# Optimization experiments

Measured on AMD Instinct MI355X. Metric: run time of the kernel, lower is better.

Reference implementation:

```python
import jax, jax.numpy as jnp
import numpy as np

V = 50000
E = 640000
DIM = 128
NUM_EDGE_TYPES = 32


def setup_inputs() -> dict:
    key = jax.random.key(0)
    ks = jax.random.split(key, 8)
    return {
        "node_values": jax.random.normal(ks[0], (V, DIM), dtype=jnp.float32),
        "edge_src": jax.random.randint(ks[1], (E,), 0, V, dtype=jnp.int32),
        "edge_dest": jax.random.randint(ks[2], (E,), 0, V, dtype=jnp.int32),
        "edge_cls": jax.random.randint(ks[3], (E,), 0, NUM_EDGE_TYPES, dtype=jnp.int32),
        "W_src": jax.random.normal(ks[4], (DIM, DIM), dtype=jnp.float32) / np.sqrt(DIM),
        "b_src": jnp.zeros((DIM,), dtype=jnp.float32),
        "W_dest": jax.random.normal(ks[5], (DIM, DIM), dtype=jnp.float32) / np.sqrt(DIM),
        "b_dest": jnp.zeros((DIM,), dtype=jnp.float32),
        "edge_emb": jax.random.normal(ks[6], (NUM_EDGE_TYPES, DIM), dtype=jnp.float32),
    }


def reference(node_values, edge_src, edge_dest, edge_cls, W_src, b_src, W_dest, b_dest, edge_emb):
    # Dense projections over all nodes, then gather per edge (matches tf.gather(dense(...), idx))
    src_proj = node_values @ W_src + b_src    # [V, dim]
    dest_proj = node_values @ W_dest + b_dest  # [V, dim]
    # Per-edge fused message: gather src, gather dest, edge-class embedding lookup, add, relu
    msgs = jax.nn.relu(src_proj[edge_src] + dest_proj[edge_dest] + edge_emb[edge_cls])  # [E, dim]
    # Scatter-reduce messages onto destination nodes
    out = jax.ops.segment_sum(msgs, edge_dest, num_segments=V)  # [V, dim]
    return out
```

## Files before the change

kernel.cpp:

```cpp
#include <hip/hip_runtime.h>


#define V 50000
#define E 640000
#define DIM 128
#define NXCD 8
#define NBIN_R 50
#define BINW 125
#define NBINS 400
#define BINCAP 2048
#define QCAP 384
#define NCHUNK 256
#define CSRN 2500
#define EC4 625
#define NPROJ 782
#define NFUSED 1038

typedef __bf16 bf16x8 __attribute__((ext_vector_type(8)));
typedef float  f32x4  __attribute__((ext_vector_type(4)));
typedef float  f32x2  __attribute__((ext_vector_type(2)));

__device__ __forceinline__ float bf2f(unsigned int u16) {
    union { unsigned int i; float f; } c; c.i = u16 << 16; return c.f;
}
__device__ __forceinline__ unsigned int f2bf(float f) {
    union { float f; unsigned int i; } c; c.f = f;
    unsigned int u = c.i;
    return (u + 0x7FFFu + ((u >> 16) & 1u)) >> 16;
}

__global__ __launch_bounds__(256) void mp_setup(
    const float* __restrict__ Ws, const float* __restrict__ Wd,
    const float* __restrict__ emb,
    unsigned short* __restrict__ Wpk, unsigned short* __restrict__ embB,
    int* __restrict__ binCnt)
{
    int tid = blockIdx.x * 256 + threadIdx.x;
    int mat  = tid >> 11;
    int rem  = tid & 2047;
    int ct   = rem >> 8;
    int kt   = (rem >> 6) & 3;
    int lane = rem & 63;
    const float* W = mat ? Wd : Ws;
    int n  = ct * 16 + (lane & 15);
    int k0 = kt * 32 + (lane >> 4) * 8;
    unsigned short* dst = Wpk + (size_t)tid * 8;
    #pragma unroll
    for (int j = 0; j < 8; ++j) dst[j] = (unsigned short)f2bf(W[(k0 + j) * DIM + n]);
    embB[tid] = (unsigned short)f2bf(emb[tid]);
    if (tid < NBINS) binCnt[tid] = 0;
}

__global__ __launch_bounds__(256) void mp_fused(
    const int* __restrict__ ed, const int* __restrict__ es, const int* __restrict__ ec,
    int* __restrict__ binCnt, int* __restrict__ binbuf,
    const float* __restrict__ x, const unsigned short* __restrict__ Wpk,
    const float* __restrict__ bs, const float* __restrict__ bd,
    unsigned char* __restrict__ ps8, unsigned short* __restrict__ pdB)
{
    __shared__ float stage[4][16 * 132];

    const int b = blockIdx.x;
    const int t = threadIdx.x;
    const bool isBin = ((b & 3) == 3) && (b < 1024);

    if (isBin) {
        int* base  = (int*)&stage[0][0];
        int* hist  = base;
        int* lofs  = base + 400;
        int* lcur  = base + 801;
        int* gbase = base + 1201;
        int* csr   = base + 1601;
        unsigned short* sbin = (unsigned short*)(base + 4101);

        const int c = b >> 2;

        for (int i = t; i < NBINS; i += 256) hist[i] = 0;

        int4 DV[3], SV[3], CV[3];
        {
            const int4* ed4 = (const int4*)ed + (size_t)c * EC4;
            const int4* es4 = (const int4*)es + (size_t)c * EC4;
            const int4* ec4 = (const int4*)ec + (size_t)c * EC4;
            #pragma unroll
            for (int k = 0; k < 3; ++k) {
                int i = t + k * 256;
                if (i < EC4) { DV[k] = ed4[i]; SV[k] = es4[i]; CV[k] = ec4[i]; }
                else { DV[k] = make_int4(-1, -1, -1, -1);
                       SV[k] = make_int4(0, 0, 0, 0); CV[k] = make_int4(0, 0, 0, 0); }
            }
        }
        __syncthreads();

        #pragma unroll
        for (int k = 0; k < 3; ++k) {
            #define H1(D) if ((D) >= 0) atomicAdd(&hist[(unsigned)(D) / BINW], 1);
            H1(DV[k].x); H1(DV[k].y); H1(DV[k].z); H1(DV[k].w);
            #undef H1
        }
        __syncthreads();

        for (int i = t; i < NBINS; i += 256)
            gbase[i] = atomicAdd(&binCnt[i], hist[i]);
        if (t < 64) {
            int carry = 0;
            #pragma unroll
            for (int s = 0; s < 7; ++s) {
                int idx = s * 64 + t;
                int v = (idx < NBINS) ? hist[idx] : 0;
                #pragma unroll
                for (int dlt = 1; dlt < 64; dlt <<= 1) {
                    int u = __shfl_up(v, dlt, 64);
                    if (t >= dlt) v += u;
                }
                int tot = __shfl(v, 63, 64);
                v += carry;
                if (idx < NBINS) { lofs[idx + 1] = v; lcur[idx] = v - hist[idx]; }
                carry += tot;
            }
            if (t == 0) lofs[0] = 0;
        }
        __syncthreads();

        #pragma unroll
        for (int k = 0; k < 3; ++k) {
            #define SC1(D, S, C) if ((D) >= 0) { \
                int bn = (unsigned)(D) / BINW; \
                int rl = (D) - bn * BINW; \
                int pos = atomicAdd(&lcur[bn], 1); \
                csr[pos] = ((S) & 0xFFFF) | ((C) << 16) | (rl << 21); \
                sbin[pos] = (unsigned short)bn; }
            SC1(DV[k].x, SV[k].x, CV[k].x); SC1(DV[k].y, SV[k].y, CV[k].y);
            SC1(DV[k].z, SV[k].z, CV[k].z); SC1(DV[k].w, SV[k].w, CV[k].w);
            #undef SC1
        }
        __syncthreads();

        for (int i = t; i < CSRN; i += 256) {
            int bb = sbin[i];
            int slot = gbase[bb] + (i - lofs[bb]);
            if (slot < BINCAP)
                binbuf[(size_t)bb * BINCAP + slot] = csr[i];
        }
        return;
    }

    const int p = (b < 1024) ? (b - ((b + 1) >> 2)) : (b - 256);
    if (p >= NPROJ) return;
    const int wave = __builtin_amdgcn_readfirstlane(threadIdx.x) >> 6;
    const int lane = threadIdx.x & 63;
    const int m = lane & 15, q = lane >> 4;
    const int row0 = p * 64 + wave * 16;

    int arow = row0 + m; if (arow >= V) arow = V - 1;
    const float* xr = x + (size_t)arow * DIM + q * 8;

    bf16x8 A[4];
    #pragma unroll
    for (int kt = 0; kt < 4; ++kt) {
        float4 u = *(const float4*)(xr + kt * 32);
        float4 v = *(const float4*)(xr + kt * 32 + 4);
        bf16x8 a;
        a[0] = (__bf16)u.x; a[1] = (__bf16)u.y; a[2] = (__bf16)u.z; a[3] = (__bf16)u.w;
        a[4] = (__bf16)v.x; a[5] = (__bf16)v.y; a[6] = (__bf16)v.z; a[7] = (__bf16)v.w;
        A[kt] = a;
    }

    const bf16x8* Bp = (const bf16x8*)Wpk;

    f32x4 accS[8], accD[8];
    #pragma unroll
    for (int ct = 0; ct < 8; ++ct) {
        f32x4 aS = {0.f, 0.f, 0.f, 0.f}, aD = {0.f, 0.f, 0.f, 0.f};
        #pragma unroll
        for (int kt = 0; kt < 4; ++kt) {
            bf16x8 bS = Bp[((0 * 8 + ct) * 4 + kt) * 64 + lane];
            bf16x8 bD = Bp[((1 * 8 + ct) * 4 + kt) * 64 + lane];
            aS = __builtin_amdgcn_mfma_f32_16x16x32_bf16(A[kt], bS, aS, 0, 0, 0);
            aD = __builtin_amdgcn_mfma_f32_16x16x32_bf16(A[kt], bD, aD, 0, 0, 0);
        }
        accS[ct] = aS; accD[ct] = aD;
    }

    float* st = stage[wave];
    const int rr = lane & 15, cg = lane >> 4;
    const int orow = row0 + rr;
    const float* rowp = st + rr * 132 + cg * 32;

    #pragma unroll
    for (int ct = 0; ct < 8; ++ct) {
        const float bv = bs[ct * 16 + m];
        #pragma unroll
        for (int rg = 0; rg < 4; ++rg)
            st[(q * 4 + rg) * 132 + ct * 16 + m] = accS[ct][rg] + bv;
    }
    __syncthreads();
    {
        int w[8];
        #pragma unroll
        for (int j = 0; j < 8; ++j) {
            float4 f = *(const float4*)(rowp + 4 * j);
            int v = __builtin_amdgcn_cvt_pk_fp8_f32(f.x, f.y, 0, false);
            v = __builtin_amdgcn_cvt_pk_fp8_f32(f.z, f.w, v, true);
            w[j] = v;
        }
        if (orow < V) {
            int4* dst = (int4*)(ps8 + (size_t)orow * 128 + cg * 32);
            dst[0] = make_int4(w[0], w[1], w[2], w[3]);
            dst[1] = make_int4(w[4], w[5], w[6], w[7]);
        }
    }
    __syncthreads();

    #pragma unroll
    for (int ct = 0; ct < 8; ++ct) {
        const float bv = bd[ct * 16 + m];
        #pragma unroll
        for (int rg = 0; rg < 4; ++rg)
            st[(q * 4 + rg) * 132 + ct * 16 + m] = accD[ct][rg] + bv;
    }
    __syncthreads();
    {
        int w[16];
        #pragma unroll
        for (int j = 0; j < 8; ++j) {
            float4 f = *(const float4*)(rowp + 4 * j);
            w[2 * j]     = f2bf(f.x) | (f2bf(f.y) << 16);
            w[2 * j + 1] = f2bf(f.z) | (f2bf(f.w) << 16);
        }
        if (orow < V) {
            int4* dst = (int4*)(pdB + (size_t)orow * 128 + cg * 32);
            #pragma unroll
            for (int jj = 0; jj < 4; ++jj)
                dst[jj] = make_int4(w[4 * jj], w[4 * jj + 1], w[4 * jj + 2], w[4 * jj + 3]);
        }
    }
}

__global__ __launch_bounds__(256) void mp_binBC(
    const unsigned char* __restrict__ ps8, const unsigned short* __restrict__ pdB,
    const unsigned short* __restrict__ embB,
    const int* __restrict__ binCnt, const int* __restrict__ binbuf,
    float* __restrict__ out)
{
    __shared__ int csr[QCAP];
    __shared__ int cnt[16];
    __shared__ int off[17];
    __shared__ int cur[16];

    const int r = blockIdx.x & (NXCD - 1);
    const int rest = blockIdx.x >> 3;
    const int bi = rest % NBIN_R;
    const int qu = rest / NBIN_R;
    const int bin = r * NBIN_R + bi;
    const int rel0 = qu * 16;
    const int relW = (qu == 7) ? 13 : 16;
    const int d0 = bin * BINW + rel0;
    const int t = threadIdx.x;
    const int wave = t >> 6, lane = t & 63;

    int nb = binCnt[bin]; if (nb > BINCAP) nb = BINCAP;
    const int* buf = binbuf + (size_t)bin * BINCAP;

    if (t < 16) cnt[t] = 0;

    int EB[8];
    #pragma unroll
    for (int k = 0; k < 8; ++k) {
        int i = t + k * 256;
        EB[k] = (i < nb) ? buf[i] : -1;
    }

    float dp0v[4], dp1v[4];
    #pragma unroll
    for (int k = 0; k < 4; ++k) {
        int rl = wave + k * 4;
        int d = d0 + ((rl < relW) ? rl : 0);
        unsigned int pdu = *(const unsigned int*)(pdB + (size_t)d * DIM + 2 * lane);
        dp0v[k] = bf2f(pdu & 0xFFFF); dp1v[k] = bf2f(pdu >> 16);
    }
    __syncthreads();

    #pragma unroll
    for (int k = 0; k < 8; ++k) {
        int rl = (int)((unsigned)EB[k] >> 21) - rel0;
        if ((unsigned)rl < (unsigned)relW) atomicAdd(&cnt[rl], 1);
    }
    __syncthreads();

    if (t < 16) {
        int v = (t < relW) ? cnt[t] : 0;
        #pragma unroll
        for (int dlt = 1; dlt < 16; dlt <<= 1) {
            int u = __shfl_up(v, dlt, 64);
            if (t >= dlt) v += u;
        }
        off[t + 1] = v;
        cur[t] = v - cnt[t];
        if (t == 0) off[0] = 0;
    }
    __syncthreads();

    #pragma unroll
    for (int k = 0; k < 8; ++k) {
        int rl = (int)((unsigned)EB[k] >> 21) - rel0;
        if ((unsigned)rl < (unsigned)relW) {
            int pos = atomicAdd(&cur[rl], 1);
            if (pos < QCAP) csr[pos] = EB[k];
        }
    }
    __syncthreads();

    #define PROC(P) { \
        int s_ = *(const unsigned short*)(ps8 + ((size_t)((P) & 0xFFFF) << 7) + 2 * lane); \
        unsigned int e_ = *(const unsigned int*)(embB + ((((P) >> 16) & 0x1F) << 7) + 2 * lane); \
        f32x2 f_ = __builtin_amdgcn_cvt_pk_f32_fp8(s_, false); \
        a0 += fmaxf(f_.x + dp0 + bf2f(e_ & 0xFFFF), 0.f); \
        a1 += fmaxf(f_.y + dp1 + bf2f(e_ >> 16),    0.f); }

    #pragma unroll
    for (int k = 0; k < 4; ++k) {
        const int rl = wave + k * 4;
        if (rl >= relW) break;
        const int d = d0 + rl;
        int i0 = off[rl], i1 = off[rl + 1];
        if (i1 > QCAP) i1 = QCAP;
        if (i0 > i1) i0 = i1;
        const float dp0 = dp0v[k], dp1 = dp1v[k];
        float a0 = 0.f, a1 = 0.f;
        int i = i0;
        for (; i + 8 <= i1; i += 8) {
            int p0 = csr[i],     p1 = csr[i + 1], p2 = csr[i + 2], p3 = csr[i + 3];
            int p4 = csr[i + 4], p5 = csr[i + 5], p6 = csr[i + 6], p7 = csr[i + 7];
            PROC(p0); PROC(p1); PROC(p2); PROC(p3);
            PROC(p4); PROC(p5); PROC(p6); PROC(p7);
        }
        for (; i + 4 <= i1; i += 4) {
            int p0 = csr[i], p1 = csr[i + 1], p2 = csr[i + 2], p3 = csr[i + 3];
            PROC(p0); PROC(p1); PROC(p2); PROC(p3);
        }
        for (; i < i1; ++i) { int p0 = csr[i]; PROC(p0); }
        *(float2*)(out + (size_t)d * DIM + 2 * lane) = make_float2(a0, a1);
    }
    #undef PROC
}

extern "C" void kernel_launch(void* const* d_in, const int* in_sizes, int n_in,
                              void* d_out, int out_size, void* d_ws, size_t ws_size,
                              hipStream_t stream) {
    const float* x   = (const float*)d_in[0];
    const int*   es  = (const int*)d_in[1];
    const int*   ed  = (const int*)d_in[2];
    const int*   ec  = (const int*)d_in[3];
    const float* Ws  = (const float*)d_in[4];
    const float* bs  = (const float*)d_in[5];
    const float* Wd  = (const float*)d_in[6];
    const float* bd  = (const float*)d_in[7];
    const float* emb = (const float*)d_in[8];
    float* out = (float*)d_out;

    char* ws = (char*)d_ws;
    size_t off = 0;
    unsigned char*  ps8  = (unsigned char*)(ws + off);  off += (size_t)V * 128;
    unsigned short* pdB  = (unsigned short*)(ws + off); off += (size_t)V * DIM * 2;
    int* binbuf = (int*)(ws + off);                     off += (size_t)NBINS * BINCAP * 4;
    int* binCnt = (int*)(ws + off);                     off += (size_t)NBINS * 4;
    unsigned short* Wpk  = (unsigned short*)(ws + off); off += 2 * 128 * 128 * 2;
    unsigned short* embB = (unsigned short*)(ws + off); off += 32 * 128 * 2;

    mp_setup<<<16, 256, 0, stream>>>(Ws, Wd, emb, Wpk, embB, binCnt);
    mp_fused<<<NFUSED, 256, 0, stream>>>(ed, es, ec, binCnt, binbuf,
                                         x, Wpk, bs, bd, ps8, pdB);
    mp_binBC<<<NBIN_R * NXCD * 8, 256, 0, stream>>>(ps8, pdB, embB, binCnt, binbuf, out);
}
```

Measured before the change: 147.5 us.

## Shrink fused kernel LDS/registers, pad bin counters, stage embeddings in LDS

The projection epilogue now runs as four 64-column passes with a per-wave LDS stage and wave-local waitcnt fences instead of block barriers. This shrinks LDS and accumulator registers so more blocks can be resident (launch_bounds 256,8). Sort blocks also take on the leftover projection tiles, bringing the grid to 1024 blocks. Global bin counters are padded to separate cache lines to reduce atomic contention, and the global atomic is moved after the prefix scan. The scatter kernel copies the edge-class embedding table into LDS once per block. The risk is correctness of the wave-only fences: they rely on each wave reading back only its own LDS region.

```diff
diff --git a/kernel.cpp b/kernel.cpp
--- a/kernel.cpp
+++ b/kernel.cpp
@@ -8,13 +8,16 @@
 #define NBIN_R 50
 #define BINW 125
 #define NBINS 400
+#define CSTRIDE 16
 #define BINCAP 2048
 #define QCAP 384
-#define NCHUNK 256
 #define CSRN 2500
 #define EC4 625
 #define NPROJ 782
-#define NFUSED 1038
+#define NFUSED 1024
+#define SQ 68
+
+#define WFENCE() asm volatile("s_waitcnt lgkmcnt(0)" ::: "memory")
 
 typedef __bf16 bf16x8 __attribute__((ext_vector_type(8)));
 typedef float  f32x4  __attribute__((ext_vector_type(4)));
@@ -48,30 +51,30 @@
     #pragma unroll
     for (int j = 0; j < 8; ++j) dst[j] = (unsigned short)f2bf(W[(k0 + j) * DIM + n]);
     embB[tid] = (unsigned short)f2bf(emb[tid]);
-    if (tid < NBINS) binCnt[tid] = 0;
-}
-
-__global__ __launch_bounds__(256) void mp_fused(
+    for (int i = tid; i < NBINS * CSTRIDE; i += 4096) binCnt[i] = 0;
+}
+
+__global__ __launch_bounds__(256, 8) void mp_fused(
     const int* __restrict__ ed, const int* __restrict__ es, const int* __restrict__ ec,
     int* __restrict__ binCnt, int* __restrict__ binbuf,
     const float* __restrict__ x, const unsigned short* __restrict__ Wpk,
     const float* __restrict__ bs, const float* __restrict__ bd,
     unsigned char* __restrict__ ps8, unsigned short* __restrict__ pdB)
 {
-    __shared__ float stage[4][16 * 132];
+    __shared__ int lds[4951];
 
     const int b = blockIdx.x;
     const int t = threadIdx.x;
-    const bool isBin = ((b & 3) == 3) && (b < 1024);
-
-    if (isBin) {
-        int* base  = (int*)&stage[0][0];
-        int* hist  = base;
-        int* lofs  = base + 400;
-        int* lcur  = base + 801;
-        int* gbase = base + 1201;
-        int* csr   = base + 1601;
-        unsigned short* sbin = (unsigned short*)(base + 4101);
+    const bool isSort = ((b & 3) == 3);
+    int p;
+
+    if (isSort) {
+        int* hist = lds;
+        int* lofs = lds + 400;
+        int* lcur = lds + 801;
+        int* csr  = lds + 1201;
+        unsigned short* sbin = (unsigned short*)(lds + 3701);
+        int* gbase = hist;
 
         const int c = b >> 2;
 
@@ -100,8 +103,6 @@
         }
         __syncthreads();
 
-        for (int i = t; i < NBINS; i += 256)
-            gbase[i] = atomicAdd(&binCnt[i], hist[i]);
         if (t < 64) {
             int carry = 0;
             #pragma unroll
@@ -122,6 +123,9 @@
         }
         __syncthreads();
 
+        for (int i = t; i < NBINS; i += 256)
+            gbase[i] = atomicAdd(&binCnt[i * CSTRIDE], hist[i]);
+
         #pragma unroll
         for (int k = 0; k < 3; ++k) {
             #define SC1(D, S, C) if ((D) >= 0) { \
@@ -142,11 +146,13 @@
             if (slot < BINCAP)
                 binbuf[(size_t)bb * BINCAP + slot] = csr[i];
         }
-        return;
-    }
-
-    const int p = (b < 1024) ? (b - ((b + 1) >> 2)) : (b - 256);
-    if (p >= NPROJ) return;
+        if (c >= 14) return;
+        __syncthreads();
+        p = 768 + c;
+    } else {
+        p = b - ((b + 1) >> 2);
+    }
+
     const int wave = __builtin_amdgcn_readfirstlane(threadIdx.x) >> 6;
     const int lane = threadIdx.x & 63;
     const int m = lane & 15, q = lane >> 4;
@@ -167,73 +173,72 @@
     }
 
     const bf16x8* Bp = (const bf16x8*)Wpk;
-
-    f32x4 accS[8], accD[8];
-    #pragma unroll
-    for (int ct = 0; ct < 8; ++ct) {
-        f32x4 aS = {0.f, 0.f, 0.f, 0.f}, aD = {0.f, 0.f, 0.f, 0.f};
-        #pragma unroll
-        for (int kt = 0; kt < 4; ++kt) {
-            bf16x8 bS = Bp[((0 * 8 + ct) * 4 + kt) * 64 + lane];
-            bf16x8 bD = Bp[((1 * 8 + ct) * 4 + kt) * 64 + lane];
-            aS = __builtin_amdgcn_mfma_f32_16x16x32_bf16(A[kt], bS, aS, 0, 0, 0);
-            aD = __builtin_amdgcn_mfma_f32_16x16x32_bf16(A[kt], bD, aD, 0, 0, 0);
-        }
-        accS[ct] = aS; accD[ct] = aD;
-    }
-
-    float* st = stage[wave];
+    float* stw = (float*)lds + wave * 1088;
     const int rr = lane & 15, cg = lane >> 4;
     const int orow = row0 + rr;
-    const float* rowp = st + rr * 132 + cg * 32;
-
-    #pragma unroll
-    for (int ct = 0; ct < 8; ++ct) {
-        const float bv = bs[ct * 16 + m];
-        #pragma unroll
-        for (int rg = 0; rg < 4; ++rg)
-            st[(q * 4 + rg) * 132 + ct * 16 + m] = accS[ct][rg] + bv;
-    }
-    __syncthreads();
-    {
-        int w[8];
-        #pragma unroll
-        for (int j = 0; j < 8; ++j) {
-            float4 f = *(const float4*)(rowp + 4 * j);
-            int v = __builtin_amdgcn_cvt_pk_fp8_f32(f.x, f.y, 0, false);
-            v = __builtin_amdgcn_cvt_pk_fp8_f32(f.z, f.w, v, true);
-            w[j] = v;
-        }
-        if (orow < V) {
-            int4* dst = (int4*)(ps8 + (size_t)orow * 128 + cg * 32);
-            dst[0] = make_int4(w[0], w[1], w[2], w[3]);
-            dst[1] = make_int4(w[4], w[5], w[6], w[7]);
-        }
-    }
-    __syncthreads();
-
-    #pragma unroll
-    for (int ct = 0; ct < 8; ++ct) {
-        const float bv = bd[ct * 16 + m];
-        #pragma unroll
-        for (int rg = 0; rg < 4; ++rg)
-            st[(q * 4 + rg) * 132 + ct * 16 + m] = accD[ct][rg] + bv;
-    }
-    __syncthreads();
-    {
-        int w[16];
-        #pragma unroll
-        for (int j = 0; j < 8; ++j) {
-            float4 f = *(const float4*)(rowp + 4 * j);
-            w[2 * j]     = f2bf(f.x) | (f2bf(f.y) << 16);
-            w[2 * j + 1] = f2bf(f.z) | (f2bf(f.w) << 16);
-        }
-        if (orow < V) {
-            int4* dst = (int4*)(pdB + (size_t)orow * 128 + cg * 32);
+    const float* rowp = stw + rr * SQ + cg * 16;
+
+    #pragma unroll
+    for (int half = 0; half < 4; ++half) {
+        const float* bias = (half < 2) ? bs : bd;
+        const int hco = (half & 1) * 64;
+
+        f32x4 acc[4];
+        #pragma unroll
+        for (int ct = 0; ct < 4; ++ct) {
+            bf16x8 B0 = Bp[(half * 16 + ct * 4 + 0) * 64 + lane];
+            bf16x8 B1 = Bp[(half * 16 + ct * 4 + 1) * 64 + lane];
+            bf16x8 B2 = Bp[(half * 16 + ct * 4 + 2) * 64 + lane];
+            bf16x8 B3 = Bp[(half * 16 + ct * 4 + 3) * 64 + lane];
+            f32x4 a = {0.f, 0.f, 0.f, 0.f};
+            a = __builtin_amdgcn_mfma_f32_16x16x32_bf16(A[0], B0, a, 0, 0, 0);
+            a = __builtin_amdgcn_mfma_f32_16x16x32_bf16(A[1], B1, a, 0, 0, 0);
+            a = __builtin_amdgcn_mfma_f32_16x16x32_bf16(A[2], B2, a, 0, 0, 0);
+            a = __builtin_amdgcn_mfma_f32_16x16x32_bf16(A[3], B3, a, 0, 0, 0);
+            acc[ct] = a;
+        }
+
+        #pragma unroll
+        for (int ct = 0; ct < 4; ++ct) {
+            const float bv = bias[hco + ct * 16 + m];
             #pragma unroll
-            for (int jj = 0; jj < 4; ++jj)
-                dst[jj] = make_int4(w[4 * jj], w[4 * jj + 1], w[4 * jj + 2], w[4 * jj + 3]);
-        }
+            for (int rg = 0; rg < 4; ++rg)
+                stw[(q * 4 + rg) * SQ + ct * 16 + m] = acc[ct][rg] + bv;
+        }
+        WFENCE();
+
+        float4 f0 = *(const float4*)(rowp + 0);
+        float4 f1 = *(const float4*)(rowp + 4);
+        float4 f2 = *(const float4*)(rowp + 8);
+        float4 f3 = *(const float4*)(rowp + 12);
+        if (half < 2) {
+            int w0 = __builtin_amdgcn_cvt_pk_fp8_f32(f0.x, f0.y, 0, false);
+            w0 = __builtin_amdgcn_cvt_pk_fp8_f32(f0.z, f0.w, w0, true);
+            int w1 = __builtin_amdgcn_cvt_pk_fp8_f32(f1.x, f1.y, 0, false);
+            w1 = __builtin_amdgcn_cvt_pk_fp8_f32(f1.z, f1.w, w1, true);
+            int w2 = __builtin_amdgcn_cvt_pk_fp8_f32(f2.x, f2.y, 0, false);
+            w2 = __builtin_amdgcn_cvt_pk_fp8_f32(f2.z, f2.w, w2, true);
+            int w3 = __builtin_amdgcn_cvt_pk_fp8_f32(f3.x, f3.y, 0, false);
+            w3 = __builtin_amdgcn_cvt_pk_fp8_f32(f3.z, f3.w, w3, true);
+            if (orow < V)
+                *(int4*)(ps8 + (size_t)orow * 128 + hco + cg * 16) =
+                    make_int4(w0, w1, w2, w3);
+        } else {
+            int u0 = f2bf(f0.x) | (f2bf(f0.y) << 16);
+            int u1 = f2bf(f0.z) | (f2bf(f0.w) << 16);
+            int u2 = f2bf(f1.x) | (f2bf(f1.y) << 16);
+            int u3 = f2bf(f1.z) | (f2bf(f1.w) << 16);
+            int u4 = f2bf(f2.x) | (f2bf(f2.y) << 16);
+            int u5 = f2bf(f2.z) | (f2bf(f2.w) << 16);
+            int u6 = f2bf(f3.x) | (f2bf(f3.y) << 16);
+            int u7 = f2bf(f3.z) | (f2bf(f3.w) << 16);
+            if (orow < V) {
+                char* dst = (char*)pdB + (size_t)orow * 256 + hco * 2 + cg * 32;
+                ((int4*)dst)[0] = make_int4(u0, u1, u2, u3);
+                ((int4*)dst)[1] = make_int4(u4, u5, u6, u7);
+            }
+        }
+        WFENCE();
     }
 }
 
@@ -247,6 +252,7 @@
     __shared__ int cnt[16];
     __shared__ int off[17];
     __shared__ int cur[16];
+    __shared__ unsigned short sEmb[32 * DIM];
 
     const int r = blockIdx.x & (NXCD - 1);
     const int rest = blockIdx.x >> 3;
@@ -259,10 +265,17 @@
     const int t = threadIdx.x;
     const int wave = t >> 6, lane = t & 63;
 
-    int nb = binCnt[bin]; if (nb > BINCAP) nb = BINCAP;
+    int nb = binCnt[bin * CSTRIDE]; if (nb > BINCAP) nb = BINCAP;
     const int* buf = binbuf + (size_t)bin * BINCAP;
 
     if (t < 16) cnt[t] = 0;
+
+    {
+        const int4* s4 = (const int4*)embB;
+        int4* d4 = (int4*)sEmb;
+        d4[t] = s4[t];
+        d4[t + 256] = s4[t + 256];
+    }
 
     int EB[8];
     #pragma unroll
@@ -313,7 +326,7 @@
 
     #define PROC(P) { \
         int s_ = *(const unsigned short*)(ps8 + ((size_t)((P) & 0xFFFF) << 7) + 2 * lane); \
-        unsigned int e_ = *(const unsigned int*)(embB + ((((P) >> 16) & 0x1F) << 7) + 2 * lane); \
+        unsigned int e_ = *(const unsigned int*)(sEmb + ((((P) >> 16) & 0x1F) << 7) + 2 * lane); \
         f32x2 f_ = __builtin_amdgcn_cvt_pk_f32_fp8(s_, false); \
         a0 += fmaxf(f_.x + dp0 + bf2f(e_ & 0xFFFF), 0.f); \
         a1 += fmaxf(f_.y + dp1 + bf2f(e_ >> 16),    0.f); }
@@ -364,12 +377,12 @@
     unsigned char*  ps8  = (unsigned char*)(ws + off);  off += (size_t)V * 128;
     unsigned short* pdB  = (unsigned short*)(ws + off); off += (size_t)V * DIM * 2;
     int* binbuf = (int*)(ws + off);                     off += (size_t)NBINS * BINCAP * 4;
-    int* binCnt = (int*)(ws + off);                     off += (size_t)NBINS * 4;
+    int* binCnt = (int*)(ws + off);                     off += (size_t)NBINS * CSTRIDE * 4;
     unsigned short* Wpk  = (unsigned short*)(ws + off); off += 2 * 128 * 128 * 2;
     unsigned short* embB = (unsigned short*)(ws + off); off += 32 * 128 * 2;
 
     mp_setup<<<16, 256, 0, stream>>>(Ws, Wd, emb, Wpk, embB, binCnt);
     mp_fused<<<NFUSED, 256, 0, stream>>>(ed, es, ec, binCnt, binbuf,
                                          x, Wpk, bs, bd, ps8, pdB);
-    mp_binBC<<<NBIN_R * NXCD * 8, 256, 0, stream>>>(ps8, pdB, embB, binCnt, binbuf, out);
-}
+    mp_binBC<<<NBINS * 8, 256, 0, stream>>>(ps8, pdB, embB, binCnt, binbuf, out);
+}
```

New measurement: 142.6 us. 1.03x faster.
